# Optimization experiments

Measured on AMD Instinct MI355X. Metric: run time of the kernel, lower is better.

The kernel has to match this reference:

```python
import math
import jax, jax.numpy as jnp
import numpy as np

NUM_POS_FEATS = 256
TEMPERATURE = 10000.0
NORMALIZE = True
SCALE = 2.0 * math.pi
POSSEG_LEN = 512
EPS = 1e-6

BSZ, L, D = 32, 8192, 256


def setup_inputs() -> dict:
    key = jax.random.key(0)
    kx, km = jax.random.split(key)
    x = jax.random.normal(kx, (BSZ, L, D), dtype=jnp.float32)
    mask = jax.random.randint(km, (BSZ, L), 0, 2, dtype=jnp.int32)
    return {"x": x, "mask": mask}


def _pos_embed(mask):
    """Vectorized segmented-cumsum sinusoidal position embedding.

    Segments of length POSSEG_LEN start at the first valid (mask==1) index of
    each row and tile to the end. Positions before the first valid index, rows
    with no valid positions, and all-zero segments produce x_embed == 0, which
    reproduces the torch default fill (sin(0)=0 at even dims, cos(0)=1 at odd).
    """
    bsz, L = mask.shape
    idx = jnp.arange(L, dtype=jnp.int32)
    valid = mask == 1
    has_valid = jnp.any(valid, axis=1)                       # (B,)
    start = jnp.argmax(valid, axis=1).astype(jnp.int32)      # (B,) first valid idx

    c = jnp.cumsum(mask, axis=1).astype(jnp.float32)         # (B, L) running count
    rel = idx[None, :] - start[:, None]                      # (B, L)
    seg_id = jnp.maximum(rel, 0) // POSSEG_LEN               # (B, L)
    seg_start = start[:, None] + seg_id * POSSEG_LEN         # (B, L)
    seg_end = jnp.minimum(seg_start + POSSEG_LEN, L)         # exclusive end

    # cumsum just before the segment start (0 if segment starts at position 0)
    c_prev = jnp.where(
        seg_start > 0,
        jnp.take_along_axis(c, jnp.maximum(seg_start - 1, 0), axis=1),
        0.0,
    )
    x_embed = c - c_prev                                     # segmented cumsum
    # cumsum value at the last element of each position's segment
    seg_last = jnp.take_along_axis(c, seg_end - 1, axis=1) - c_prev

    in_range = (rel >= 0) & has_valid[:, None]
    x_embed = jnp.where(in_range, x_embed, 0.0)

    if NORMALIZE:
        x_embed = x_embed / (seg_last + EPS) * SCALE

    dim_t = jnp.arange(NUM_POS_FEATS, dtype=jnp.float32)
    dim_t = TEMPERATURE ** (2.0 * jnp.floor(dim_t / 2.0) / NUM_POS_FEATS)

    pos = x_embed[..., None] / dim_t                         # (B, L, F)
    # interleave sin(even dims) and cos(odd dims)
    out = jnp.stack(
        [jnp.sin(pos[..., 0::2]), jnp.cos(pos[..., 1::2])], axis=-1
    ).reshape(bsz, L, NUM_POS_FEATS)
    return out


def reference(x, mask):
    return _pos_embed(mask)
```

## Files before the change

### kernel.cpp

```cpp
#include <hip/hip_runtime.h>
#include <hip/hip_bf16.h>

#define L_LEN   8192
#define SEG     512
#define NFEATS  256
#define SCALE_2PI 6.283185307179586f
#define EPS_REF 1e-6f

#define STEP_LOG2 0.1038102529652301f

__global__ __launch_bounds__(256) void pe_phase1(const int* __restrict__ mask,
                                                 float* __restrict__ xe) {
    constexpr int THREADS = 256;
    constexpr int CHUNK = L_LEN / THREADS;

    __shared__ int c[L_LEN];
    __shared__ int partials[THREADS];
    __shared__ int firstIdx;

    const int t = threadIdx.x;
    const int b = blockIdx.x;
    const int* mrow = mask + (long)b * L_LEN;

    if (t == 0) firstIdx = L_LEN;
    __syncthreads();

    int m[CHUNK];
    const int base = t * CHUNK;
    const int4* mv = (const int4*)(mrow + base);
#pragma unroll
    for (int j = 0; j < CHUNK / 4; ++j) {
        int4 v = mv[j];
        m[4 * j + 0] = v.x; m[4 * j + 1] = v.y;
        m[4 * j + 2] = v.z; m[4 * j + 3] = v.w;
    }

    int s = 0;
    int lf = L_LEN;
#pragma unroll
    for (int j = 0; j < CHUNK; ++j) {
        if (m[j] != 0 && lf == L_LEN) lf = base + j;
        s += m[j];
    }
    partials[t] = s;
    if (lf < L_LEN) atomicMin(&firstIdx, lf);
    __syncthreads();

    for (int off = 1; off < THREADS; off <<= 1) {
        int v = partials[t];
        int add = (t >= off) ? partials[t - off] : 0;
        __syncthreads();
        partials[t] = v + add;
        __syncthreads();
    }

    int run = partials[t] - s;
#pragma unroll
    for (int j = 0; j < CHUNK; ++j) {
        run += m[j];
        c[base + j] = run;
    }
    __syncthreads();

    const int start = firstIdx;
    const bool hv = (start < L_LEN);
    float* xrow = xe + (long)b * L_LEN;

#pragma unroll
    for (int j = 0; j < CHUNK; ++j) {
        const int i = base + j;
        float e = 0.0f;
        const int rel = i - start;
        if (hv && rel >= 0) {
            const int seg_start = start + (rel / SEG) * SEG;
            const int seg_end = min(seg_start + SEG, L_LEN);
            const int cprev = (seg_start > 0) ? c[seg_start - 1] : 0;
            const int ci = c[i];
            const int clast = c[seg_end - 1];
            e = (float)(ci - cprev) / ((float)(clast - cprev) + EPS_REF) * SCALE_2PI;
        }
        xrow[i] = e;
    }
}

__global__ __launch_bounds__(256) void pe_phase2(const float* __restrict__ xe,
                                                 float4* __restrict__ out) {
    const int lane = threadIdx.x & 63;
    const int wave = threadIdx.x >> 6;

    const float inv0 = exp2f(-(float)(2 * lane) * STEP_LOG2);
    const float inv1 = exp2f(-(float)(2 * lane + 1) * STEP_LOG2);

    const int p0 = blockIdx.x * 16 + wave * 4;
#pragma unroll
    for (int j = 0; j < 4; ++j) {
        const int p = p0 + j;
        const float e = xe[p];
        const float t0 = e * inv0;
        const float t1 = e * inv1;
        float s0, c0, s1, c1;
        __sincosf(t0, &s0, &c0);
        __sincosf(t1, &s1, &c1);
        out[(long)p * (NFEATS / 4) + lane] = make_float4(s0, c0, s1, c1);
    }
}

extern "C" void kernel_launch(void* const* d_in, const int* in_sizes, int n_in,
                              void* d_out, int out_size, void* d_ws, size_t ws_size,
                              hipStream_t stream) {
    const int* mask = (const int*)d_in[1];
    float* out = (float*)d_out;
    float* xe = (float*)d_ws;

    const int B = in_sizes[1] / L_LEN;
    const int npos = B * L_LEN;

    pe_phase1<<<dim3(B), dim3(256), 0, stream>>>(mask, xe);
    pe_phase2<<<dim3(npos / 16), dim3(256), 0, stream>>>(xe, (float4*)out);
}
```

Before: 385.8 us.

## Use native sin/cos builtins, nontemporal stores, larger per-thread work, skewed LDS

New measurement: 387.2 us. Within noise of the previous version (+0.4%).

```diff
diff --git a/kernel.cpp b/kernel.cpp
--- a/kernel.cpp
+++ b/kernel.cpp
@@ -4,17 +4,20 @@
 #define L_LEN   8192
 #define SEG     512
 #define NFEATS  256
-#define SCALE_2PI 6.283185307179586f
 #define EPS_REF 1e-6f
 
 #define STEP_LOG2 0.1038102529652301f
+
+typedef float vfloat4 __attribute__((ext_vector_type(4)));
+
+__device__ __forceinline__ int skew(int i) { return i + (i >> 5); }
 
 __global__ __launch_bounds__(256) void pe_phase1(const int* __restrict__ mask,
                                                  float* __restrict__ xe) {
     constexpr int THREADS = 256;
     constexpr int CHUNK = L_LEN / THREADS;
 
-    __shared__ int c[L_LEN];
+    __shared__ int c[L_LEN + (L_LEN >> 5)];
     __shared__ int partials[THREADS];
     __shared__ int firstIdx;
 
@@ -58,7 +61,7 @@
 #pragma unroll
     for (int j = 0; j < CHUNK; ++j) {
         run += m[j];
-        c[base + j] = run;
+        c[skew(base + j)] = run;
     }
     __syncthreads();
 
@@ -72,36 +75,36 @@
         float e = 0.0f;
         const int rel = i - start;
         if (hv && rel >= 0) {
-            const int seg_start = start + (rel / SEG) * SEG;
+            const int seg_start = start + (rel >> 9) * SEG;
             const int seg_end = min(seg_start + SEG, L_LEN);
-            const int cprev = (seg_start > 0) ? c[seg_start - 1] : 0;
-            const int ci = c[i];
-            const int clast = c[seg_end - 1];
-            e = (float)(ci - cprev) / ((float)(clast - cprev) + EPS_REF) * SCALE_2PI;
+            const int cprev = (seg_start > 0) ? c[skew(seg_start - 1)] : 0;
+            const int ci = c[skew(i)];
+            const int clast = c[skew(seg_end - 1)];
+            e = (float)(ci - cprev) / ((float)(clast - cprev) + EPS_REF);
         }
         xrow[i] = e;
     }
 }
 
 __global__ __launch_bounds__(256) void pe_phase2(const float* __restrict__ xe,
-                                                 float4* __restrict__ out) {
+                                                 vfloat4* __restrict__ out) {
     const int lane = threadIdx.x & 63;
     const int wave = threadIdx.x >> 6;
 
     const float inv0 = exp2f(-(float)(2 * lane) * STEP_LOG2);
     const float inv1 = exp2f(-(float)(2 * lane + 1) * STEP_LOG2);
 
-    const int p0 = blockIdx.x * 16 + wave * 4;
+    const int p0 = blockIdx.x * 32 + wave * 8;
 #pragma unroll
-    for (int j = 0; j < 4; ++j) {
+    for (int j = 0; j < 8; ++j) {
         const int p = p0 + j;
         const float e = xe[p];
-        const float t0 = e * inv0;
-        const float t1 = e * inv1;
-        float s0, c0, s1, c1;
-        __sincosf(t0, &s0, &c0);
-        __sincosf(t1, &s1, &c1);
-        out[(long)p * (NFEATS / 4) + lane] = make_float4(s0, c0, s1, c1);
+        vfloat4 r;
+        r.x = __builtin_amdgcn_sinf(e * inv0);
+        r.y = __builtin_amdgcn_cosf(e * inv0);
+        r.z = __builtin_amdgcn_sinf(e * inv1);
+        r.w = __builtin_amdgcn_cosf(e * inv1);
+        __builtin_nontemporal_store(r, &out[(long)p * (NFEATS / 4) + lane]);
     }
 }
 
@@ -109,12 +112,12 @@
                               void* d_out, int out_size, void* d_ws, size_t ws_size,
                               hipStream_t stream) {
     const int* mask = (const int*)d_in[1];
-    float* out = (float*)d_out;
+    vfloat4* out = (vfloat4*)d_out;
     float* xe = (float*)d_ws;
 
     const int B = in_sizes[1] / L_LEN;
     const int npos = B * L_LEN;
 
     pe_phase1<<<dim3(B), dim3(256), 0, stream>>>(mask, xe);
-    pe_phase2<<<dim3(npos / 16), dim3(256), 0, stream>>>(xe, (float4*)out);
+    pe_phase2<<<dim3(npos / 32), dim3(256), 0, stream>>>(xe, out);
 }
```
